# Performance work log

Measured on AMD Instinct MI355X. Metric: run time of the kernel, lower is better.

Reference implementation:

```python
import jax, jax.numpy as jnp
import numpy as np

DIM = 1024          # hidden_size
MOE_HID = 512       # moe_intermediate_size
SHARED_HID = 2048   # shared_expert_intermediate_size
N_EXPERTS = 16
TOP_K = 2
NORM_TOPK_PROB = True


def setup_inputs() -> dict:
    key = jax.random.key(0)
    ks = jax.random.split(key, 9)
    s = 0.02  # init scale
    x = jax.random.normal(ks[0], (2, 1024, DIM), dtype=jnp.float32)
    Wg = jax.random.normal(ks[1], (N_EXPERTS, DIM), dtype=jnp.float32) * s
    We_gate = jax.random.normal(ks[2], (N_EXPERTS, MOE_HID, DIM), dtype=jnp.float32) * s
    We_up = jax.random.normal(ks[3], (N_EXPERTS, MOE_HID, DIM), dtype=jnp.float32) * s
    We_down = jax.random.normal(ks[4], (N_EXPERTS, DIM, MOE_HID), dtype=jnp.float32) * s
    Ws_gate = jax.random.normal(ks[5], (SHARED_HID, DIM), dtype=jnp.float32) * s
    Ws_up = jax.random.normal(ks[6], (SHARED_HID, DIM), dtype=jnp.float32) * s
    Ws_down = jax.random.normal(ks[7], (DIM, SHARED_HID), dtype=jnp.float32) * s
    Wsg = jax.random.normal(ks[8], (1, DIM), dtype=jnp.float32) * s
    return {"x": x, "Wg": Wg, "We_gate": We_gate, "We_up": We_up,
            "We_down": We_down, "Ws_gate": Ws_gate, "Ws_up": Ws_up,
            "Ws_down": Ws_down, "Wsg": Wsg}


def reference(x, Wg, We_gate, We_up, We_down, Ws_gate, Ws_up, Ws_down, Wsg):
    B, S, D = x.shape
    xt = x.reshape(-1, D)  # [T, D] tokens
    # router: softmax over experts, then top-k
    gates = jax.nn.softmax(xt @ Wg.T, axis=-1)          # [T, E]
    scores, inds = jax.lax.top_k(gates, TOP_K)           # [T, K]
    if NORM_TOPK_PROB:
        scores = scores / jnp.sum(scores, axis=-1, keepdims=True)
    # experts: SwiGLU computed for all experts, then gather the top-k outputs
    g = jnp.einsum('td,ehd->teh', xt, We_gate)           # [T, E, H]
    u = jnp.einsum('td,ehd->teh', xt, We_up)             # [T, E, H]
    h = jax.nn.silu(g) * u                               # swiglu
    y_all = jnp.einsum('teh,edh->ted', h, We_down)       # [T, E, D]
    y_sel = jnp.take_along_axis(y_all, inds[:, :, None], axis=1)  # [T, K, D]
    y = jnp.sum(y_sel * scores[:, :, None], axis=1)      # [T, D]
    # shared expert with sigmoid gate
    shared = (jax.nn.silu(xt @ Ws_gate.T) * (xt @ Ws_up.T)) @ Ws_down.T  # [T, D]
    y = y + jax.nn.sigmoid(xt @ Wsg.T) * shared
    return y.reshape(B, S, D)
```

## Files before the change

### kernel.cpp

```cpp
#include <hip/hip_runtime.h>
#include <stdint.h>

#define DIM 1024
#define MOE_HID 512
#define SH_HID 2048
#define NE 16
#define NT 2048
#define ROWS_CAP 6144

typedef unsigned short u16;
typedef __attribute__((ext_vector_type(8))) short s16x8;
typedef __attribute__((ext_vector_type(4))) float f32x4;

#define SYNC_BAR() \
  asm volatile("s_waitcnt lgkmcnt(0)" ::: "memory"); \
  __builtin_amdgcn_sched_barrier(0); \
  __builtin_amdgcn_s_barrier(); \
  __builtin_amdgcn_sched_barrier(0);

__device__ __forceinline__ u16 f2bf(float f){
  union { float f; unsigned v; } x; x.f = f;
  unsigned r = x.v + 0x7FFF + ((x.v >> 16) & 1);
  return (u16)(r >> 16);
}

__device__ __forceinline__ s16x8 cvt8pk(float4 a, float4 b){
  union { s16x8 v; unsigned u[4]; } r;
  asm volatile("v_cvt_pk_bf16_f32 %0, %1, %2" : "=v"(r.u[0]) : "v"(a.x), "v"(a.y));
  asm volatile("v_cvt_pk_bf16_f32 %0, %1, %2" : "=v"(r.u[1]) : "v"(a.z), "v"(a.w));
  asm volatile("v_cvt_pk_bf16_f32 %0, %1, %2" : "=v"(r.u[2]) : "v"(b.x), "v"(b.y));
  asm volatile("v_cvt_pk_bf16_f32 %0, %1, %2" : "=v"(r.u[3]) : "v"(b.z), "v"(b.w));
  return r.v;
}

__global__ void k_cvt_x(const float* __restrict__ s, u16* __restrict__ d){
  int i = (blockIdx.x * 256 + threadIdx.x) * 4;
  float4 v = *(const float4*)(s + i);
  ushort4 o;
  o.x = f2bf(v.x); o.y = f2bf(v.y); o.z = f2bf(v.z); o.w = f2bf(v.w);
  *(ushort4*)(d + i) = o;
}

__global__ void k_router(const float* __restrict__ x, const float* __restrict__ Wg,
                         const float* __restrict__ Wsgate1,
                         int* __restrict__ inds, float* __restrict__ scores,
                         float* __restrict__ gl){
  int lane = threadIdx.x & 63;
  int t = blockIdx.x * 4 + (threadIdx.x >> 6);
  const float4* xt = (const float4*)(x + (size_t)t * DIM);
  float4 xv[4];
#pragma unroll
  for(int j = 0; j < 4; j++) xv[j] = xt[lane + 64 * j];

  float acc[NE + 1];
#pragma unroll
  for(int e = 0; e <= NE; e++) acc[e] = 0.f;

#pragma unroll
  for(int e = 0; e < NE; e++){
    const float4* wr = (const float4*)(Wg + (size_t)e * DIM);
#pragma unroll
    for(int j = 0; j < 4; j++){
      float4 w = wr[lane + 64 * j];
      acc[e] += xv[j].x * w.x + xv[j].y * w.y + xv[j].z * w.z + xv[j].w * w.w;
    }
  }
  {
    const float4* wr = (const float4*)Wsgate1;
#pragma unroll
    for(int j = 0; j < 4; j++){
      float4 w = wr[lane + 64 * j];
      acc[NE] += xv[j].x * w.x + xv[j].y * w.y + xv[j].z * w.z + xv[j].w * w.w;
    }
  }

#pragma unroll
  for(int off = 32; off; off >>= 1)
#pragma unroll
    for(int e = 0; e <= NE; e++) acc[e] += __shfl_xor(acc[e], off, 64);

  if(lane == 0){
    int b0 = 0; float v0 = acc[0];
    for(int e = 1; e < NE; e++) if(acc[e] > v0){ v0 = acc[e]; b0 = e; }
    int b1 = (b0 == 0) ? 1 : 0; float v1 = acc[b1];
    for(int e = 0; e < NE; e++) if(e != b0 && acc[e] > v1){ v1 = acc[e]; b1 = e; }
    float s0 = 1.f / (1.f + __expf(v1 - v0));
    inds[t*2+0] = b0; inds[t*2+1] = b1;
    scores[t*2+0] = s0; scores[t*2+1] = 1.f - s0;
    gl[t] = acc[NE];
  }
}

__global__ void k_assign(const int* __restrict__ inds, const float* __restrict__ scores,
                         int* __restrict__ counts, int* __restrict__ offs,
                         int* __restrict__ rowinfo, float* __restrict__ rowscore){
  __shared__ int cnt[NE], off_s[NE], fill[NE];
  int tid = threadIdx.x;
  if(tid < NE){ cnt[tid] = 0; fill[tid] = 0; }
  __syncthreads();
  int ea[4];
#pragma unroll
  for(int i = 0; i < 4; i++){
    int a = tid + 1024 * i;
    ea[i] = inds[a];
    atomicAdd(&cnt[ea[i]], 1);
  }
  __syncthreads();
  if(tid == 0){
    int o = 0;
    for(int e = 0; e < NE; e++){
      off_s[e] = o;
      o += (cnt[e] + 127) & ~127;
    }
  }
  __syncthreads();
#pragma unroll
  for(int i = 0; i < 4; i++){
    int a = tid + 1024 * i;
    int e = ea[i];
    int row = off_s[e] + atomicAdd(&fill[e], 1);
    rowinfo[row] = a;
    rowscore[row] = scores[a];
  }
  if(tid < NE){ counts[tid] = cnt[tid]; offs[tid] = off_s[tid]; }
}

__global__ __launch_bounds__(256, 2) void k_gateup_exp(
    const u16* __restrict__ xb, const int* __restrict__ rowinfo,
    const float* __restrict__ Weg, const float* __restrict__ Weu,
    u16* __restrict__ Hm,
    const int* __restrict__ counts, const int* __restrict__ offs){
  __shared__ __align__(16) u16 As[2][128 * 64];
  __shared__ __align__(16) u16 Bgs[2][64 * 64];
  __shared__ __align__(16) u16 Bus[2][64 * 64];

  const int row0 = blockIdx.y * 128;
  const int n0 = blockIdx.x * 64;
  const int rows_used = offs[NE-1] + ((counts[NE-1] + 127) & ~127);
  if(row0 >= rows_used) return;
  int e = 0;
#pragma unroll
  for(int k = 1; k < NE; k++) if(row0 >= offs[k]) e = k;

  const float* Bg = Weg + (size_t)e * MOE_HID * DIM + (size_t)n0 * DIM;
  const float* Bu = Weu + (size_t)e * MOE_HID * DIM + (size_t)n0 * DIM;
  u16* H = Hm + (size_t)row0 * MOE_HID + n0;

  const int tid = threadIdx.x, lane = tid & 63, wid = tid >> 6;
  const int wm = wid >> 1, wn = wid & 1;
  const int srow = tid >> 2;
  const int p16 = (tid & 3) * 16;
  const int cb = (tid & 3) * 2;
  const int key = srow & 7;
  const int fr = lane & 15;
  const int fc = lane >> 4;
  const int fx = fr & 7;

  const int wA00 = (srow     ) * 64 + ((cb    ) ^ key) * 8;
  const int wA01 = (srow     ) * 64 + ((cb + 1) ^ key) * 8;
  const int wA10 = (srow + 64) * 64 + ((cb    ) ^ key) * 8;
  const int wA11 = (srow + 64) * 64 + ((cb + 1) ^ key) * 8;
  const int wB0  = srow * 64 + ((cb    ) ^ key) * 8;
  const int wB1  = srow * 64 + ((cb + 1) ^ key) * 8;

  int a0 = rowinfo[row0 + srow];
  int a1 = rowinfo[row0 + 64 + srow];
  int t0 = ((unsigned)a0 < 4096u) ? (a0 >> 1) : 0;
  int t1 = ((unsigned)a1 < 4096u) ? (a1 >> 1) : 0;
  const u16* Ar0 = xb + (size_t)t0 * DIM + p16;
  const u16* Ar1 = xb + (size_t)t1 * DIM + p16;
  const float* Bgr = Bg + (size_t)srow * DIM + p16;
  const float* Bur = Bu + (size_t)srow * DIM + p16;

  uint4 aE00, aE01, aE10, aE11, aO00, aO01, aO10, aO11;
  float4 gE0, gE1, gE2, gE3, uE0, uE1, uE2, uE3;
  float4 gO0, gO1, gO2, gO3, uO0, uO1, uO2, uO3;

#define GX_LOAD(S, ko) \
  a##S##00 = *(const uint4*)(Ar0 + (ko));      a##S##01 = *(const uint4*)(Ar0 + (ko) + 8); \
  a##S##10 = *(const uint4*)(Ar1 + (ko));      a##S##11 = *(const uint4*)(Ar1 + (ko) + 8); \
  g##S##0 = *(const float4*)(Bgr + (ko));      g##S##1 = *(const float4*)(Bgr + (ko) + 4); \
  g##S##2 = *(const float4*)(Bgr + (ko) + 8);  g##S##3 = *(const float4*)(Bgr + (ko) + 12); \
  u##S##0 = *(const float4*)(Bur + (ko));      u##S##1 = *(const float4*)(Bur + (ko) + 4); \
  u##S##2 = *(const float4*)(Bur + (ko) + 8);  u##S##3 = *(const float4*)(Bur + (ko) + 12);

  f32x4 accg[4][2], accu[4][2];
#pragma unroll
  for(int m = 0; m < 4; m++)
#pragma unroll
    for(int n = 0; n < 2; n++){
      accg[m][n] = (f32x4){0.f,0.f,0.f,0.f};
      accu[m][n] = (f32x4){0.f,0.f,0.f,0.f};
    }

  GX_LOAD(E, 0)
  GX_LOAD(O, 64)

#define GX_STEP(tt, S, bb) { \
  *(uint4*)(As[bb] + wA00) = a##S##00; \
  *(uint4*)(As[bb] + wA01) = a##S##01; \
  *(uint4*)(As[bb] + wA10) = a##S##10; \
  *(uint4*)(As[bb] + wA11) = a##S##11; \
  *(s16x8*)(Bgs[bb] + wB0) = cvt8pk(g##S##0, g##S##1); \
  *(s16x8*)(Bgs[bb] + wB1) = cvt8pk(g##S##2, g##S##3); \
  *(s16x8*)(Bus[bb] + wB0) = cvt8pk(u##S##0, u##S##1); \
  *(s16x8*)(Bus[bb] + wB1) = cvt8pk(u##S##2, u##S##3); \
  SYNC_BAR() \
  if((tt) + 2 < 16){ GX_LOAD(S, ((tt) + 2) * 64) } \
  s16x8 af[4][2], bgf[2][2], buf2[2][2]; \
  _Pragma("unroll") for(int m = 0; m < 4; m++){ \
    int r = wm*64 + m*16 + fr; \
    _Pragma("unroll") for(int ks = 0; ks < 2; ks++) \
      af[m][ks] = *(const s16x8*)(As[bb] + r*64 + (((ks*4 + fc) ^ fx)) * 8); } \
  _Pragma("unroll") for(int n = 0; n < 2; n++){ \
    int r = wn*32 + n*16 + fr; \
    _Pragma("unroll") for(int ks = 0; ks < 2; ks++){ \
      bgf[n][ks]  = *(const s16x8*)(Bgs[bb] + r*64 + (((ks*4 + fc) ^ fx)) * 8); \
      buf2[n][ks] = *(const s16x8*)(Bus[bb] + r*64 + (((ks*4 + fc) ^ fx)) * 8); } } \
  _Pragma("unroll") for(int m = 0; m < 4; m++) \
  _Pragma("unroll") for(int n = 0; n < 2; n++){ \
    accg[m][n] = __builtin_amdgcn_mfma_f32_16x16x32_bf16(af[m][0], bgf[n][0], accg[m][n], 0, 0, 0); \
    accg[m][n] = __builtin_amdgcn_mfma_f32_16x16x32_bf16(af[m][1], bgf[n][1], accg[m][n], 0, 0, 0); \
    accu[m][n] = __builtin_amdgcn_mfma_f32_16x16x32_bf16(af[m][0], buf2[n][0], accu[m][n], 0, 0, 0); \
    accu[m][n] = __builtin_amdgcn_mfma_f32_16x16x32_bf16(af[m][1], buf2[n][1], accu[m][n], 0, 0, 0); } }

  for(int t = 0; t < 16; t += 2){
    GX_STEP(t,     E, 0)
    GX_STEP(t + 1, O, 1)
  }

#pragma unroll
  for(int m = 0; m < 4; m++)
#pragma unroll
    for(int n = 0; n < 2; n++)
#pragma unroll
      for(int i = 0; i < 4; i++){
        int r = wm*64 + m*16 + ((lane >> 4) << 2) + i;
        int c = wn*32 + n*16 + (lane & 15);
        float g = accg[m][n][i], u = accu[m][n][i];
        float h = (g / (1.f + __expf(-g))) * u;
        H[(size_t)r * MOE_HID + c] = f2bf(h);
      }
}

__global__ __launch_bounds__(256, 2) void k_gateup_sh(
    const u16* __restrict__ xb,
    const float* __restrict__ Wsg, const float* __restrict__ Wsu,
    u16* __restrict__ Hs){
  __shared__ __align__(16) u16 As[2][256 * 32];
  __shared__ __align__(16) u16 Bgs[2][64 * 32];
  __shared__ __align__(16) u16 Bus[2][64 * 32];

  const int mtile = blockIdx.y;
  const int n0 = blockIdx.x * 64;

  const u16* A = xb + (size_t)mtile * 256 * DIM;
  const float* Bg = Wsg + (size_t)n0 * DIM;
  const float* Bu = Wsu + (size_t)n0 * DIM;
  u16* H = Hs + (size_t)mtile * 256 * SH_HID + n0;

  const int tid = threadIdx.x, lane = tid & 63, wid = tid >> 6;
  const int wm = wid >> 1, wn = wid & 1;
  const int srow = tid >> 2, p8 = (tid & 3) * 8;
  const int swz8 = (((tid & 3) ^ ((tid >> 3) & 3))) * 8;
  const int fr = lane & 15;
  const int fkswz = (((lane >> 4) ^ ((lane >> 1) & 3))) * 8;
  const int wA0 = (srow      ) * 32 + swz8;
  const int wA1 = (srow +  64) * 32 + swz8;
  const int wA2 = (srow + 128) * 32 + swz8;
  const int wA3 = (srow + 192) * 32 + swz8;
  const int wB  = srow * 32 + swz8;

  const u16* Ar0 = A + (size_t)(srow      ) * DIM + p8;
  const u16* Ar1 = A + (size_t)(srow +  64) * DIM + p8;
  const u16* Ar2 = A + (size_t)(srow + 128) * DIM + p8;
  const u16* Ar3 = A + (size_t)(srow + 192) * DIM + p8;
  const float* Bgr = Bg + (size_t)srow * DIM + p8;
  const float* Bur = Bu + (size_t)srow * DIM + p8;

  uint4 aE0,aE1,aE2,aE3, aO0,aO1,aO2,aO3;
  float4 gE0,gE1,uE0,uE1, gO0,gO1,uO0,uO1;

#define GS_LOAD(S, ko) \
  a##S##0 = *(const uint4*)(Ar0 + (ko)); a##S##1 = *(const uint4*)(Ar1 + (ko)); \
  a##S##2 = *(const uint4*)(Ar2 + (ko)); a##S##3 = *(const uint4*)(Ar3 + (ko)); \
  g##S##0 = *(const float4*)(Bgr + (ko)); g##S##1 = *(const float4*)(Bgr + (ko) + 4); \
  u##S##0 = *(const float4*)(Bur + (ko)); u##S##1 = *(const float4*)(Bur + (ko) + 4);

  f32x4 accg[8][2], accu[8][2];
#pragma unroll
  for(int m = 0; m < 8; m++)
#pragma unroll
    for(int n = 0; n < 2; n++){
      accg[m][n] = (f32x4){0.f,0.f,0.f,0.f};
      accu[m][n] = (f32x4){0.f,0.f,0.f,0.f};
    }

  GS_LOAD(E, 0)
  GS_LOAD(O, 32)

#define GS_STEP(tt, S, bb) { \
  *(uint4*)(As[bb] + wA0) = a##S##0; \
  *(uint4*)(As[bb] + wA1) = a##S##1; \
  *(uint4*)(As[bb] + wA2) = a##S##2; \
  *(uint4*)(As[bb] + wA3) = a##S##3; \
  *(s16x8*)(Bgs[bb] + wB) = cvt8pk(g##S##0, g##S##1); \
  *(s16x8*)(Bus[bb] + wB) = cvt8pk(u##S##0, u##S##1); \
  SYNC_BAR() \
  if((tt) + 2 < 32){ GS_LOAD(S, ((tt) + 2) * 32) } \
  s16x8 af[8], bgf[2], buf2[2]; \
  _Pragma("unroll") for(int m = 0; m < 8; m++) \
    af[m] = *(const s16x8*)(As[bb] + (wm*128 + m*16 + fr) * 32 + fkswz); \
  _Pragma("unroll") for(int n = 0; n < 2; n++){ \
    bgf[n]  = *(const s16x8*)(Bgs[bb] + (wn*32 + n*16 + fr) * 32 + fkswz); \
    buf2[n] = *(const s16x8*)(Bus[bb] + (wn*32 + n*16 + fr) * 32 + fkswz); } \
  _Pragma("unroll") for(int m = 0; m < 8; m++) \
  _Pragma("unroll") for(int n = 0; n < 2; n++){ \
    accg[m][n] = __builtin_amdgcn_mfma_f32_16x16x32_bf16(af[m], bgf[n], accg[m][n], 0, 0, 0); \
    accu[m][n] = __builtin_amdgcn_mfma_f32_16x16x32_bf16(af[m], buf2[n], accu[m][n], 0, 0, 0); } }

  for(int t = 0; t < 32; t += 2){
    GS_STEP(t,     E, 0)
    GS_STEP(t + 1, O, 1)
  }

#pragma unroll
  for(int m = 0; m < 8; m++)
#pragma unroll
    for(int n = 0; n < 2; n++)
#pragma unroll
      for(int i = 0; i < 4; i++){
        int r = wm*128 + m*16 + ((lane >> 4) << 2) + i;
        int c = wn*32 + n*16 + (lane & 15);
        float g = accg[m][n][i], u = accu[m][n][i];
        float h = (g / (1.f + __expf(-g))) * u;
        H[(size_t)r * SH_HID + c] = f2bf(h);
      }
}

__global__ __launch_bounds__(256, 2) void k_down_all(
    const u16* __restrict__ Hm, const u16* __restrict__ Hs,
    const float* __restrict__ Wed, const float* __restrict__ Wsd,
    float* __restrict__ yp, float* __restrict__ Sh0, float* __restrict__ Sh1,
    const int* __restrict__ counts, const int* __restrict__ offs,
    const int* __restrict__ rowinfo, const float* __restrict__ rowscore){
  __shared__ __align__(16) u16 As[2][128 * 32];
  __shared__ __align__(16) u16 Bs[2][128 * 32];

  const int y = blockIdx.y, n0 = blockIdx.x * 128;
  const bool sh = (y < 32);
  const u16* A; const float* B; float* O = yp;
  int lda, M = NT, row0 = 0, kBeg = 0, nk, lrow = 0;
  if(sh){
    int mtile = y & 15, kz = y >> 4;
    A = Hs + (size_t)mtile * 128 * SH_HID; lda = SH_HID;
    B = Wsd; kBeg = kz * 1024; nk = 32;
    O = (kz == 0) ? Sh0 : Sh1;
    row0 = mtile * 128;
  } else {
    row0 = (y - 32) * 128;
    int rows_used = offs[NE-1] + ((counts[NE-1] + 127) & ~127);
    if(row0 >= rows_used) return;
    int e = 0;
#pragma unroll
    for(int k = 1; k < NE; k++) if(row0 >= offs[k]) e = k;
    M = counts[e];
    lrow = row0 - offs[e];
    A = Hm + (size_t)row0 * MOE_HID; lda = MOE_HID;
    B = Wed + (size_t)e * DIM * MOE_HID; nk = 16;
  }

  const int tid = threadIdx.x, lane = tid & 63, wid = tid >> 6;
  const int wm = wid >> 1, wn = wid & 1;
  const int srow = tid >> 2, p8 = (tid & 3) * 8;
  const int swz8 = (((tid & 3) ^ ((tid >> 3) & 3))) * 8;
  const int fr = lane & 15;
  const int fkswz = (((lane >> 4) ^ ((lane >> 1) & 3))) * 8;
  const int wA0 = srow * 32 + swz8, wA1 = (64 + srow) * 32 + swz8;

  const u16* Ar0 = A + (size_t)srow * lda + kBeg + p8;
  const u16* Ar1 = A + (size_t)(64 + srow) * lda + kBeg + p8;
  const float* Br0 = B + (size_t)(n0 + srow) * lda + kBeg + p8;
  const float* Br1 = B + (size_t)(n0 + 64 + srow) * lda + kBeg + p8;

  uint4 aE0, aE1, aO0, aO1;
  float4 bE00, bE01, bE10, bE11, bO00, bO01, bO10, bO11;

#define DN_LOAD(S, ko) \
  a##S##0 = *(const uint4*)(Ar0 + (ko));   a##S##1 = *(const uint4*)(Ar1 + (ko)); \
  b##S##00 = *(const float4*)(Br0 + (ko)); b##S##01 = *(const float4*)(Br0 + (ko) + 4); \
  b##S##10 = *(const float4*)(Br1 + (ko)); b##S##11 = *(const float4*)(Br1 + (ko) + 4);

  f32x4 acc[4][4];
#pragma unroll
  for(int m = 0; m < 4; m++)
#pragma unroll
    for(int n = 0; n < 4; n++) acc[m][n] = (f32x4){0.f,0.f,0.f,0.f};

  DN_LOAD(E, 0)
  DN_LOAD(O, 32)

#define DN_STEP(tt, S, bb) { \
  *(uint4*)(As[bb] + wA0) = a##S##0; \
  *(uint4*)(As[bb] + wA1) = a##S##1; \
  *(s16x8*)(Bs[bb] + wA0) = cvt8pk(b##S##00, b##S##01); \
  *(s16x8*)(Bs[bb] + wA1) = cvt8pk(b##S##10, b##S##11); \
  SYNC_BAR() \
  if((tt) + 2 < nk){ DN_LOAD(S, ((tt) + 2) * 32) } \
  s16x8 af[4], bf[4]; \
  _Pragma("unroll") for(int m = 0; m < 4; m++) \
    af[m] = *(const s16x8*)(As[bb] + (wm*64 + m*16 + fr) * 32 + fkswz); \
  _Pragma("unroll") for(int n = 0; n < 4; n++) \
    bf[n] = *(const s16x8*)(Bs[bb] + (wn*64 + n*16 + fr) * 32 + fkswz); \
  _Pragma("unroll") for(int m = 0; m < 4; m++) \
  _Pragma("unroll") for(int n = 0; n < 4; n++) \
    acc[m][n] = __builtin_amdgcn_mfma_f32_16x16x32_bf16(af[m], bf[n], acc[m][n], 0, 0, 0); }

  for(int t = 0; t < nk; t += 2){
    DN_STEP(t,     E, 0)
    DN_STEP(t + 1, O, 1)
  }

#pragma unroll
  for(int m = 0; m < 4; m++)
#pragma unroll
    for(int i = 0; i < 4; i++){
      int rl = wm*64 + m*16 + ((lane >> 4) << 2) + i;
      if(sh){
        float* orow = O + (size_t)(row0 + rl) * DIM + n0 + wn*64 + (lane & 15);
#pragma unroll
        for(int n = 0; n < 4; n++) orow[n*16] = acc[m][n][i];
      } else if(lrow + rl < M){
        int ar = row0 + rl;
        int slot = rowinfo[ar];
        float sc = rowscore[ar];
        float* orow = yp + (size_t)slot * DIM + n0 + wn*64 + (lane & 15);
#pragma unroll
        for(int n = 0; n < 4; n++) orow[n*16] = sc * acc[m][n][i];
      }
    }
}

__global__ void k_combine(const float* __restrict__ yp, const float* __restrict__ Sh0,
                          const float* __restrict__ Sh1,
                          const float* __restrict__ gl, float* __restrict__ out){
  int idx = (blockIdx.x * 256 + threadIdx.x) * 4;
  int t = idx >> 10;
  float s = 1.f / (1.f + __expf(-gl[t]));
  float4 a = *(const float4*)(yp + (size_t)(t*2)   * DIM + (idx & 1023));
  float4 b = *(const float4*)(yp + (size_t)(t*2+1) * DIM + (idx & 1023));
  float4 c0 = *(const float4*)(Sh0 + idx);
  float4 c1 = *(const float4*)(Sh1 + idx);
  float4 o;
  o.x = a.x + b.x + s * (c0.x + c1.x);
  o.y = a.y + b.y + s * (c0.y + c1.y);
  o.z = a.z + b.z + s * (c0.z + c1.z);
  o.w = a.w + b.w + s * (c0.w + c1.w);
  *(float4*)(out + idx) = o;
}

extern "C" void kernel_launch(void* const* d_in, const int* in_sizes, int n_in,
                              void* d_out, int out_size, void* d_ws, size_t ws_size,
                              hipStream_t stream){
  const float* x    = (const float*)d_in[0];
  const float* Wg   = (const float*)d_in[1];
  const float* Weg  = (const float*)d_in[2];
  const float* Weu  = (const float*)d_in[3];
  const float* Wed  = (const float*)d_in[4];
  const float* Wsg  = (const float*)d_in[5];
  const float* Wsu  = (const float*)d_in[6];
  const float* Wsd  = (const float*)d_in[7];
  const float* Wg1  = (const float*)d_in[8];
  float* out = (float*)d_out;

  char* p = (char*)d_ws;
  int* inds   = (int*)p;  p += 4096 * 4;
  float* scores = (float*)p; p += 4096 * 4;
  float* gl   = (float*)p;  p += NT * 4;
  int* counts = (int*)p;  p += 64;
  int* offs   = (int*)p;  p += 64;
  int* rowinfo = (int*)p; p += ROWS_CAP * 4;
  float* rowscore = (float*)p; p += ROWS_CAP * 4;
  u16* xb     = (u16*)p;  p += (size_t)NT * DIM * 2;
  u16* Hs     = (u16*)p;  p += (size_t)NT * SH_HID * 2;
  float* Sh0  = (float*)p; p += (size_t)NT * DIM * 4;
  float* Sh1  = (float*)p; p += (size_t)NT * DIM * 4;
  u16* Hm     = (u16*)p;  p += (size_t)ROWS_CAP * MOE_HID * 2;
  float* yp   = (float*)p; p += (size_t)NT * 2 * DIM * 4;

  k_router<<<NT/4, 256, 0, stream>>>(x, Wg, Wg1, inds, scores, gl);
  k_cvt_x<<<NT * DIM / (256 * 4), 256, 0, stream>>>(x, xb);
  k_assign<<<1, 1024, 0, stream>>>(inds, scores, counts, offs, rowinfo, rowscore);

  k_gateup_exp<<<dim3(8, 48), 256, 0, stream>>>(xb, rowinfo, Weg, Weu, Hm, counts, offs);
  k_gateup_sh<<<dim3(32, 8), 256, 0, stream>>>(xb, Wsg, Wsu, Hs);
  k_down_all<<<dim3(8, 80), 256, 0, stream>>>(Hm, Hs, Wed, Wsd,
                                              yp, Sh0, Sh1, counts, offs,
                                              rowinfo, rowscore);

  k_combine<<<2048, 256, 0, stream>>>(yp, Sh0, Sh1, gl, out);
}
```

Before: 123.1 us.

## Retile shared gate/up GEMM to 128-row tiles with K=64 stages

The shared-expert gate/up kernel now uses 128x64 output tiles instead of 256x64 and a 64-wide K step with an XOR swizzle over 8 chunks. The grid grows from 256 to 512 blocks. The aim is better occupancy and CU fill from smaller accumulators, and half as many barriers per K. The cost is that each shared weight tile is loaded and converted from fp32 twice as often, and per-stage register staging grows.

Measured after the change: 121.7 us. Within noise of the previous version (-1.1%).

```diff
diff --git a/kernel.cpp b/kernel.cpp
--- a/kernel.cpp
+++ b/kernel.cpp
@@ -247,90 +247,103 @@
     const u16* __restrict__ xb,
     const float* __restrict__ Wsg, const float* __restrict__ Wsu,
     u16* __restrict__ Hs){
-  __shared__ __align__(16) u16 As[2][256 * 32];
-  __shared__ __align__(16) u16 Bgs[2][64 * 32];
-  __shared__ __align__(16) u16 Bus[2][64 * 32];
-
-  const int mtile = blockIdx.y;
+  __shared__ __align__(16) u16 As[2][128 * 64];
+  __shared__ __align__(16) u16 Bgs[2][64 * 64];
+  __shared__ __align__(16) u16 Bus[2][64 * 64];
+
+  const int row0 = blockIdx.y * 128;
   const int n0 = blockIdx.x * 64;
 
-  const u16* A = xb + (size_t)mtile * 256 * DIM;
   const float* Bg = Wsg + (size_t)n0 * DIM;
   const float* Bu = Wsu + (size_t)n0 * DIM;
-  u16* H = Hs + (size_t)mtile * 256 * SH_HID + n0;
+  u16* H = Hs + (size_t)row0 * SH_HID + n0;
 
   const int tid = threadIdx.x, lane = tid & 63, wid = tid >> 6;
   const int wm = wid >> 1, wn = wid & 1;
-  const int srow = tid >> 2, p8 = (tid & 3) * 8;
-  const int swz8 = (((tid & 3) ^ ((tid >> 3) & 3))) * 8;
+  const int srow = tid >> 2;
+  const int p16 = (tid & 3) * 16;
+  const int cb = (tid & 3) * 2;
+  const int key = srow & 7;
   const int fr = lane & 15;
-  const int fkswz = (((lane >> 4) ^ ((lane >> 1) & 3))) * 8;
-  const int wA0 = (srow      ) * 32 + swz8;
-  const int wA1 = (srow +  64) * 32 + swz8;
-  const int wA2 = (srow + 128) * 32 + swz8;
-  const int wA3 = (srow + 192) * 32 + swz8;
-  const int wB  = srow * 32 + swz8;
-
-  const u16* Ar0 = A + (size_t)(srow      ) * DIM + p8;
-  const u16* Ar1 = A + (size_t)(srow +  64) * DIM + p8;
-  const u16* Ar2 = A + (size_t)(srow + 128) * DIM + p8;
-  const u16* Ar3 = A + (size_t)(srow + 192) * DIM + p8;
-  const float* Bgr = Bg + (size_t)srow * DIM + p8;
-  const float* Bur = Bu + (size_t)srow * DIM + p8;
-
-  uint4 aE0,aE1,aE2,aE3, aO0,aO1,aO2,aO3;
-  float4 gE0,gE1,uE0,uE1, gO0,gO1,uO0,uO1;
-
-#define GS_LOAD(S, ko) \
-  a##S##0 = *(const uint4*)(Ar0 + (ko)); a##S##1 = *(const uint4*)(Ar1 + (ko)); \
-  a##S##2 = *(const uint4*)(Ar2 + (ko)); a##S##3 = *(const uint4*)(Ar3 + (ko)); \
-  g##S##0 = *(const float4*)(Bgr + (ko)); g##S##1 = *(const float4*)(Bgr + (ko) + 4); \
-  u##S##0 = *(const float4*)(Bur + (ko)); u##S##1 = *(const float4*)(Bur + (ko) + 4);
-
-  f32x4 accg[8][2], accu[8][2];
-#pragma unroll
-  for(int m = 0; m < 8; m++)
+  const int fc = lane >> 4;
+  const int fx = fr & 7;
+
+  const int wA00 = (srow     ) * 64 + ((cb    ) ^ key) * 8;
+  const int wA01 = (srow     ) * 64 + ((cb + 1) ^ key) * 8;
+  const int wA10 = (srow + 64) * 64 + ((cb    ) ^ key) * 8;
+  const int wA11 = (srow + 64) * 64 + ((cb + 1) ^ key) * 8;
+  const int wB0  = srow * 64 + ((cb    ) ^ key) * 8;
+  const int wB1  = srow * 64 + ((cb + 1) ^ key) * 8;
+
+  const u16* Ar0 = xb + (size_t)(row0 + srow) * DIM + p16;
+  const u16* Ar1 = xb + (size_t)(row0 + 64 + srow) * DIM + p16;
+  const float* Bgr = Bg + (size_t)srow * DIM + p16;
+  const float* Bur = Bu + (size_t)srow * DIM + p16;
+
+  uint4 aE00, aE01, aE10, aE11, aO00, aO01, aO10, aO11;
+  float4 gE0, gE1, gE2, gE3, uE0, uE1, uE2, uE3;
+  float4 gO0, gO1, gO2, gO3, uO0, uO1, uO2, uO3;
+
+#define GH_LOAD(S, ko) \
+  a##S##00 = *(const uint4*)(Ar0 + (ko));      a##S##01 = *(const uint4*)(Ar0 + (ko) + 8); \
+  a##S##10 = *(const uint4*)(Ar1 + (ko));      a##S##11 = *(const uint4*)(Ar1 + (ko) + 8); \
+  g##S##0 = *(const float4*)(Bgr + (ko));      g##S##1 = *(const float4*)(Bgr + (ko) + 4); \
+  g##S##2 = *(const float4*)(Bgr + (ko) + 8);  g##S##3 = *(const float4*)(Bgr + (ko) + 12); \
+  u##S##0 = *(const float4*)(Bur + (ko));      u##S##1 = *(const float4*)(Bur + (ko) + 4); \
+  u##S##2 = *(const float4*)(Bur + (ko) + 8);  u##S##3 = *(const float4*)(Bur + (ko) + 12);
+
+  f32x4 accg[4][2], accu[4][2];
+#pragma unroll
+  for(int m = 0; m < 4; m++)
 #pragma unroll
     for(int n = 0; n < 2; n++){
       accg[m][n] = (f32x4){0.f,0.f,0.f,0.f};
       accu[m][n] = (f32x4){0.f,0.f,0.f,0.f};
     }
 
-  GS_LOAD(E, 0)
-  GS_LOAD(O, 32)
-
-#define GS_STEP(tt, S, bb) { \
-  *(uint4*)(As[bb] + wA0) = a##S##0; \
-  *(uint4*)(As[bb] + wA1) = a##S##1; \
-  *(uint4*)(As[bb] + wA2) = a##S##2; \
-  *(uint4*)(As[bb] + wA3) = a##S##3; \
-  *(s16x8*)(Bgs[bb] + wB) = cvt8pk(g##S##0, g##S##1); \
-  *(s16x8*)(Bus[bb] + wB) = cvt8pk(u##S##0, u##S##1); \
+  GH_LOAD(E, 0)
+  GH_LOAD(O, 64)
+
+#define GH_STEP(tt, S, bb) { \
+  *(uint4*)(As[bb] + wA00) = a##S##00; \
+  *(uint4*)(As[bb] + wA01) = a##S##01; \
+  *(uint4*)(As[bb] + wA10) = a##S##10; \
+  *(uint4*)(As[bb] + wA11) = a##S##11; \
+  *(s16x8*)(Bgs[bb] + wB0) = cvt8pk(g##S##0, g##S##1); \
+  *(s16x8*)(Bgs[bb] + wB1) = cvt8pk(g##S##2, g##S##3); \
+  *(s16x8*)(Bus[bb] + wB0) = cvt8pk(u##S##0, u##S##1); \
+  *(s16x8*)(Bus[bb] + wB1) = cvt8pk(u##S##2, u##S##3); \
   SYNC_BAR() \
-  if((tt) + 2 < 32){ GS_LOAD(S, ((tt) + 2) * 32) } \
-  s16x8 af[8], bgf[2], buf2[2]; \
-  _Pragma("unroll") for(int m = 0; m < 8; m++) \
-    af[m] = *(const s16x8*)(As[bb] + (wm*128 + m*16 + fr) * 32 + fkswz); \
+  if((tt) + 2 < 16){ GH_LOAD(S, ((tt) + 2) * 64) } \
+  s16x8 af[4][2], bgf[2][2], buf2[2][2]; \
+  _Pragma("unroll") for(int m = 0; m < 4; m++){ \
+    int r = wm*64 + m*16 + fr; \
+    _Pragma("unroll") for(int ks = 0; ks < 2; ks++) \
+      af[m][ks] = *(const s16x8*)(As[bb] + r*64 + (((ks*4 + fc) ^ fx)) * 8); } \
   _Pragma("unroll") for(int n = 0; n < 2; n++){ \
-    bgf[n]  = *(const s16x8*)(Bgs[bb] + (wn*32 + n*16 + fr) * 32 + fkswz); \
-    buf2[n] = *(const s16x8*)(Bus[bb] + (wn*32 + n*16 + fr) * 32 + fkswz); } \
-  _Pragma("unroll") for(int m = 0; m < 8; m++) \
+    int r = wn*32 + n*16 + fr; \
+    _Pragma("unroll") for(int ks = 0; ks < 2; ks++){ \
+      bgf[n][ks]  = *(const s16x8*)(Bgs[bb] + r*64 + (((ks*4 + fc) ^ fx)) * 8); \
+      buf2[n][ks] = *(const s16x8*)(Bus[bb] + r*64 + (((ks*4 + fc) ^ fx)) * 8); } } \
+  _Pragma("unroll") for(int m = 0; m < 4; m++) \
   _Pragma("unroll") for(int n = 0; n < 2; n++){ \
-    accg[m][n] = __builtin_amdgcn_mfma_f32_16x16x32_bf16(af[m], bgf[n], accg[m][n], 0, 0, 0); \
-    accu[m][n] = __builtin_amdgcn_mfma_f32_16x16x32_bf16(af[m], buf2[n], accu[m][n], 0, 0, 0); } }
-
-  for(int t = 0; t < 32; t += 2){
-    GS_STEP(t,     E, 0)
-    GS_STEP(t + 1, O, 1)
-  }
-
-#pragma unroll
-  for(int m = 0; m < 8; m++)
+    accg[m][n] = __builtin_amdgcn_mfma_f32_16x16x32_bf16(af[m][0], bgf[n][0], accg[m][n], 0, 0, 0); \
+    accg[m][n] = __builtin_amdgcn_mfma_f32_16x16x32_bf16(af[m][1], bgf[n][1], accg[m][n], 0, 0, 0); \
+    accu[m][n] = __builtin_amdgcn_mfma_f32_16x16x32_bf16(af[m][0], buf2[n][0], accu[m][n], 0, 0, 0); \
+    accu[m][n] = __builtin_amdgcn_mfma_f32_16x16x32_bf16(af[m][1], buf2[n][1], accu[m][n], 0, 0, 0); } }
+
+  for(int t = 0; t < 16; t += 2){
+    GH_STEP(t,     E, 0)
+    GH_STEP(t + 1, O, 1)
+  }
+
+#pragma unroll
+  for(int m = 0; m < 4; m++)
 #pragma unroll
     for(int n = 0; n < 2; n++)
 #pragma unroll
       for(int i = 0; i < 4; i++){
-        int r = wm*128 + m*16 + ((lane >> 4) << 2) + i;
+        int r = wm*64 + m*16 + ((lane >> 4) << 2) + i;
         int c = wn*32 + n*16 + (lane & 15);
         float g = accg[m][n][i], u = accu[m][n][i];
         float h = (g / (1.f + __expf(-g))) * u;
@@ -493,7 +506,7 @@
   k_assign<<<1, 1024, 0, stream>>>(inds, scores, counts, offs, rowinfo, rowscore);
 
   k_gateup_exp<<<dim3(8, 48), 256, 0, stream>>>(xb, rowinfo, Weg, Weu, Hm, counts, offs);
-  k_gateup_sh<<<dim3(32, 8), 256, 0, stream>>>(xb, Wsg, Wsu, Hs);
+  k_gateup_sh<<<dim3(32, 16), 256, 0, stream>>>(xb, Wsg, Wsu, Hs);
   k_down_all<<<dim3(8, 80), 256, 0, stream>>>(Hm, Hs, Wed, Wsd,
                                               yp, Sh0, Sh1, counts, offs,
                                               rowinfo, rowscore);
```

## Fuse expert and shared-expert gate/up GEMMs into one launch

Applied to the files above, without the earlier changes.

Merges the routed-expert gate/up kernel and the shared-expert gate/up kernel into a single launch with 896 blocks. The first 384 blocks handle expert rows and the rest handle shared-expert tiles. Shared tiles change from 256x64 with K-step 32 to 128x64 with K-step 64. This removes a kernel launch and lets the two GEMMs fill the GPU together instead of the shared GEMM's 256 blocks running alone. The trade is that each shared-expert block now reuses weights across fewer rows, and blocks with early-exit empty expert rows sit in the same grid.

New measurement: 115.6 us. -6.1%, faster.

```diff
diff --git a/kernel.cpp b/kernel.cpp
--- a/kernel.cpp
+++ b/kernel.cpp
@@ -125,27 +125,17 @@
   if(tid < NE){ counts[tid] = cnt[tid]; offs[tid] = off_s[tid]; }
 }
 
-__global__ __launch_bounds__(256, 2) void k_gateup_exp(
+__global__ __launch_bounds__(256, 2) void k_gateup_fused(
     const u16* __restrict__ xb, const int* __restrict__ rowinfo,
     const float* __restrict__ Weg, const float* __restrict__ Weu,
-    u16* __restrict__ Hm,
+    const float* __restrict__ Wsg, const float* __restrict__ Wsu,
+    u16* __restrict__ Hm, u16* __restrict__ Hs,
     const int* __restrict__ counts, const int* __restrict__ offs){
   __shared__ __align__(16) u16 As[2][128 * 64];
   __shared__ __align__(16) u16 Bgs[2][64 * 64];
   __shared__ __align__(16) u16 Bus[2][64 * 64];
 
-  const int row0 = blockIdx.y * 128;
-  const int n0 = blockIdx.x * 64;
-  const int rows_used = offs[NE-1] + ((counts[NE-1] + 127) & ~127);
-  if(row0 >= rows_used) return;
-  int e = 0;
-#pragma unroll
-  for(int k = 1; k < NE; k++) if(row0 >= offs[k]) e = k;
-
-  const float* Bg = Weg + (size_t)e * MOE_HID * DIM + (size_t)n0 * DIM;
-  const float* Bu = Weu + (size_t)e * MOE_HID * DIM + (size_t)n0 * DIM;
-  u16* H = Hm + (size_t)row0 * MOE_HID + n0;
-
+  const int bid = blockIdx.x;
   const int tid = threadIdx.x, lane = tid & 63, wid = tid >> 6;
   const int wm = wid >> 1, wn = wid & 1;
   const int srow = tid >> 2;
@@ -163,20 +153,46 @@
   const int wB0  = srow * 64 + ((cb    ) ^ key) * 8;
   const int wB1  = srow * 64 + ((cb + 1) ^ key) * 8;
 
-  int a0 = rowinfo[row0 + srow];
-  int a1 = rowinfo[row0 + 64 + srow];
-  int t0 = ((unsigned)a0 < 4096u) ? (a0 >> 1) : 0;
-  int t1 = ((unsigned)a1 < 4096u) ? (a1 >> 1) : 0;
-  const u16* Ar0 = xb + (size_t)t0 * DIM + p16;
-  const u16* Ar1 = xb + (size_t)t1 * DIM + p16;
-  const float* Bgr = Bg + (size_t)srow * DIM + p16;
-  const float* Bur = Bu + (size_t)srow * DIM + p16;
+  const u16 *Ar0, *Ar1;
+  const float *Bgr, *Bur;
+  u16* H; int ldh;
+
+  if(bid < 384){
+    const int row0 = (bid >> 3) * 128;
+    const int n0 = (bid & 7) * 64;
+    const int rows_used = offs[NE-1] + ((counts[NE-1] + 127) & ~127);
+    if(row0 >= rows_used) return;
+    int e = 0;
+#pragma unroll
+    for(int k = 1; k < NE; k++) if(row0 >= offs[k]) e = k;
+
+    int a0 = rowinfo[row0 + srow];
+    int a1 = rowinfo[row0 + 64 + srow];
+    int t0 = ((unsigned)a0 < 4096u) ? (a0 >> 1) : 0;
+    int t1 = ((unsigned)a1 < 4096u) ? (a1 >> 1) : 0;
+    Ar0 = xb + (size_t)t0 * DIM + p16;
+    Ar1 = xb + (size_t)t1 * DIM + p16;
+    Bgr = Weg + (size_t)e * MOE_HID * DIM + (size_t)((bid & 7) * 64 + srow) * DIM + p16;
+    Bur = Weu + (size_t)e * MOE_HID * DIM + (size_t)((bid & 7) * 64 + srow) * DIM + p16;
+    H = Hm + (size_t)row0 * MOE_HID + n0;
+    ldh = MOE_HID;
+  } else {
+    const int i = bid - 384;
+    const int row0 = (i >> 5) * 128;
+    const int n0 = (i & 31) * 64;
+    Ar0 = xb + (size_t)(row0 + srow) * DIM + p16;
+    Ar1 = xb + (size_t)(row0 + 64 + srow) * DIM + p16;
+    Bgr = Wsg + (size_t)(n0 + srow) * DIM + p16;
+    Bur = Wsu + (size_t)(n0 + srow) * DIM + p16;
+    H = Hs + (size_t)row0 * SH_HID + n0;
+    ldh = SH_HID;
+  }
 
   uint4 aE00, aE01, aE10, aE11, aO00, aO01, aO10, aO11;
   float4 gE0, gE1, gE2, gE3, uE0, uE1, uE2, uE3;
   float4 gO0, gO1, gO2, gO3, uO0, uO1, uO2, uO3;
 
-#define GX_LOAD(S, ko) \
+#define GF_LOAD(S, ko) \
   a##S##00 = *(const uint4*)(Ar0 + (ko));      a##S##01 = *(const uint4*)(Ar0 + (ko) + 8); \
   a##S##10 = *(const uint4*)(Ar1 + (ko));      a##S##11 = *(const uint4*)(Ar1 + (ko) + 8); \
   g##S##0 = *(const float4*)(Bgr + (ko));      g##S##1 = *(const float4*)(Bgr + (ko) + 4); \
@@ -193,10 +209,10 @@
       accu[m][n] = (f32x4){0.f,0.f,0.f,0.f};
     }
 
-  GX_LOAD(E, 0)
-  GX_LOAD(O, 64)
-
-#define GX_STEP(tt, S, bb) { \
+  GF_LOAD(E, 0)
+  GF_LOAD(O, 64)
+
+#define GF_STEP(tt, S, bb) { \
   *(uint4*)(As[bb] + wA00) = a##S##00; \
   *(uint4*)(As[bb] + wA01) = a##S##01; \
   *(uint4*)(As[bb] + wA10) = a##S##10; \
@@ -206,7 +222,7 @@
   *(s16x8*)(Bus[bb] + wB0) = cvt8pk(u##S##0, u##S##1); \
   *(s16x8*)(Bus[bb] + wB1) = cvt8pk(u##S##2, u##S##3); \
   SYNC_BAR() \
-  if((tt) + 2 < 16){ GX_LOAD(S, ((tt) + 2) * 64) } \
+  if((tt) + 2 < 16){ GF_LOAD(S, ((tt) + 2) * 64) } \
   s16x8 af[4][2], bgf[2][2], buf2[2][2]; \
   _Pragma("unroll") for(int m = 0; m < 4; m++){ \
     int r = wm*64 + m*16 + fr; \
@@ -225,8 +241,8 @@
     accu[m][n] = __builtin_amdgcn_mfma_f32_16x16x32_bf16(af[m][1], buf2[n][1], accu[m][n], 0, 0, 0); } }
 
   for(int t = 0; t < 16; t += 2){
-    GX_STEP(t,     E, 0)
-    GX_STEP(t + 1, O, 1)
+    GF_STEP(t,     E, 0)
+    GF_STEP(t + 1, O, 1)
   }
 
 #pragma unroll
@@ -239,102 +255,7 @@
         int c = wn*32 + n*16 + (lane & 15);
         float g = accg[m][n][i], u = accu[m][n][i];
         float h = (g / (1.f + __expf(-g))) * u;
-        H[(size_t)r * MOE_HID + c] = f2bf(h);
-      }
-}
-
-__global__ __launch_bounds__(256, 2) void k_gateup_sh(
-    const u16* __restrict__ xb,
-    const float* __restrict__ Wsg, const float* __restrict__ Wsu,
-    u16* __restrict__ Hs){
-  __shared__ __align__(16) u16 As[2][256 * 32];
-  __shared__ __align__(16) u16 Bgs[2][64 * 32];
-  __shared__ __align__(16) u16 Bus[2][64 * 32];
-
-  const int mtile = blockIdx.y;
-  const int n0 = blockIdx.x * 64;
-
-  const u16* A = xb + (size_t)mtile * 256 * DIM;
-  const float* Bg = Wsg + (size_t)n0 * DIM;
-  const float* Bu = Wsu + (size_t)n0 * DIM;
-  u16* H = Hs + (size_t)mtile * 256 * SH_HID + n0;
-
-  const int tid = threadIdx.x, lane = tid & 63, wid = tid >> 6;
-  const int wm = wid >> 1, wn = wid & 1;
-  const int srow = tid >> 2, p8 = (tid & 3) * 8;
-  const int swz8 = (((tid & 3) ^ ((tid >> 3) & 3))) * 8;
-  const int fr = lane & 15;
-  const int fkswz = (((lane >> 4) ^ ((lane >> 1) & 3))) * 8;
-  const int wA0 = (srow      ) * 32 + swz8;
-  const int wA1 = (srow +  64) * 32 + swz8;
-  const int wA2 = (srow + 128) * 32 + swz8;
-  const int wA3 = (srow + 192) * 32 + swz8;
-  const int wB  = srow * 32 + swz8;
-
-  const u16* Ar0 = A + (size_t)(srow      ) * DIM + p8;
-  const u16* Ar1 = A + (size_t)(srow +  64) * DIM + p8;
-  const u16* Ar2 = A + (size_t)(srow + 128) * DIM + p8;
-  const u16* Ar3 = A + (size_t)(srow + 192) * DIM + p8;
-  const float* Bgr = Bg + (size_t)srow * DIM + p8;
-  const float* Bur = Bu + (size_t)srow * DIM + p8;
-
-  uint4 aE0,aE1,aE2,aE3, aO0,aO1,aO2,aO3;
-  float4 gE0,gE1,uE0,uE1, gO0,gO1,uO0,uO1;
-
-#define GS_LOAD(S, ko) \
-  a##S##0 = *(const uint4*)(Ar0 + (ko)); a##S##1 = *(const uint4*)(Ar1 + (ko)); \
-  a##S##2 = *(const uint4*)(Ar2 + (ko)); a##S##3 = *(const uint4*)(Ar3 + (ko)); \
-  g##S##0 = *(const float4*)(Bgr + (ko)); g##S##1 = *(const float4*)(Bgr + (ko) + 4); \
-  u##S##0 = *(const float4*)(Bur + (ko)); u##S##1 = *(const float4*)(Bur + (ko) + 4);
-
-  f32x4 accg[8][2], accu[8][2];
-#pragma unroll
-  for(int m = 0; m < 8; m++)
-#pragma unroll
-    for(int n = 0; n < 2; n++){
-      accg[m][n] = (f32x4){0.f,0.f,0.f,0.f};
-      accu[m][n] = (f32x4){0.f,0.f,0.f,0.f};
-    }
-
-  GS_LOAD(E, 0)
-  GS_LOAD(O, 32)
-
-#define GS_STEP(tt, S, bb) { \
-  *(uint4*)(As[bb] + wA0) = a##S##0; \
-  *(uint4*)(As[bb] + wA1) = a##S##1; \
-  *(uint4*)(As[bb] + wA2) = a##S##2; \
-  *(uint4*)(As[bb] + wA3) = a##S##3; \
-  *(s16x8*)(Bgs[bb] + wB) = cvt8pk(g##S##0, g##S##1); \
-  *(s16x8*)(Bus[bb] + wB) = cvt8pk(u##S##0, u##S##1); \
-  SYNC_BAR() \
-  if((tt) + 2 < 32){ GS_LOAD(S, ((tt) + 2) * 32) } \
-  s16x8 af[8], bgf[2], buf2[2]; \
-  _Pragma("unroll") for(int m = 0; m < 8; m++) \
-    af[m] = *(const s16x8*)(As[bb] + (wm*128 + m*16 + fr) * 32 + fkswz); \
-  _Pragma("unroll") for(int n = 0; n < 2; n++){ \
-    bgf[n]  = *(const s16x8*)(Bgs[bb] + (wn*32 + n*16 + fr) * 32 + fkswz); \
-    buf2[n] = *(const s16x8*)(Bus[bb] + (wn*32 + n*16 + fr) * 32 + fkswz); } \
-  _Pragma("unroll") for(int m = 0; m < 8; m++) \
-  _Pragma("unroll") for(int n = 0; n < 2; n++){ \
-    accg[m][n] = __builtin_amdgcn_mfma_f32_16x16x32_bf16(af[m], bgf[n], accg[m][n], 0, 0, 0); \
-    accu[m][n] = __builtin_amdgcn_mfma_f32_16x16x32_bf16(af[m], buf2[n], accu[m][n], 0, 0, 0); } }
-
-  for(int t = 0; t < 32; t += 2){
-    GS_STEP(t,     E, 0)
-    GS_STEP(t + 1, O, 1)
-  }
-
-#pragma unroll
-  for(int m = 0; m < 8; m++)
-#pragma unroll
-    for(int n = 0; n < 2; n++)
-#pragma unroll
-      for(int i = 0; i < 4; i++){
-        int r = wm*128 + m*16 + ((lane >> 4) << 2) + i;
-        int c = wn*32 + n*16 + (lane & 15);
-        float g = accg[m][n][i], u = accu[m][n][i];
-        float h = (g / (1.f + __expf(-g))) * u;
-        H[(size_t)r * SH_HID + c] = f2bf(h);
+        H[(size_t)r * ldh + c] = f2bf(h);
       }
 }
 
@@ -492,8 +413,8 @@
   k_cvt_x<<<NT * DIM / (256 * 4), 256, 0, stream>>>(x, xb);
   k_assign<<<1, 1024, 0, stream>>>(inds, scores, counts, offs, rowinfo, rowscore);
 
-  k_gateup_exp<<<dim3(8, 48), 256, 0, stream>>>(xb, rowinfo, Weg, Weu, Hm, counts, offs);
-  k_gateup_sh<<<dim3(32, 8), 256, 0, stream>>>(xb, Wsg, Wsu, Hs);
+  k_gateup_fused<<<896, 256, 0, stream>>>(xb, rowinfo, Weg, Weu, Wsg, Wsu,
+                                          Hm, Hs, counts, offs);
   k_down_all<<<dim3(8, 80), 256, 0, stream>>>(Hm, Hs, Wed, Wsd,
                                               yp, Sh0, Sh1, counts, offs,
                                               rowinfo, rowscore);
```
